# Kernel optimization log

Measured on AMD Instinct MI355X. Metric: run time of the kernel, lower is better.

The kernel has to match this reference:

```python
import jax, jax.numpy as jnp
import numpy as np

EPS = 1e-06


def rotation_trick(e, q):
    # e, q: (..., D). Faithful to torch version, but r_rT @ e and
    # q_hat_e_hatT @ e are algebraically simplified to r*(r.e) and
    # q_hat*(e_hat.e), avoiding the (..., D, D) outer-product tensors.
    sg = jax.lax.stop_gradient
    e_norm = sg(jnp.linalg.norm(e, axis=-1, keepdims=True)) + EPS
    q_norm = sg(jnp.linalg.norm(q, axis=-1, keepdims=True)) + EPS
    e_hat = sg(e / e_norm)
    q_hat = sg(q / q_norm)
    lmbda = q_norm / e_norm
    r = e_hat + q_hat
    r = r / jnp.linalg.norm(r, axis=-1, keepdims=True)
    r_dot_e = jnp.sum(r * e, axis=-1, keepdims=True)
    ehat_dot_e = jnp.sum(e_hat * e, axis=-1, keepdims=True)
    return lmbda * (e - 2.0 * r * r_dot_e + 2.0 * q_hat * ehat_dot_e)


def setup_inputs() -> dict:
    key = jax.random.key(0)
    k1, k2 = jax.random.split(key)
    B, D, H, W = 8, 64, 32, 32
    K = 8192
    x = jax.random.normal(k1, (B, D, H, W), dtype=jnp.float32)
    # init_tensor: L2-normalize uniform rand along dim=1, scale=1
    e = jax.random.uniform(k2, (D, K), dtype=jnp.float32)
    e_i_ts = e / (jnp.linalg.norm(e, axis=1, keepdims=True) + 1e-12)
    return {"x": x, "e_i_ts": e_i_ts}


def reference(x, e_i_ts):
    # x: (B, D, H, W); e_i_ts: (D, K)
    B, D, H, W = x.shape
    x_perm = jnp.transpose(x, (0, 2, 3, 1))          # (B, H, W, D)
    flat_x = x_perm.reshape(-1, D)                   # (N, D)
    distances = (
        jnp.sum(flat_x**2, axis=1, keepdims=True)
        - 2.0 * flat_x @ e_i_ts
        + jnp.sum(e_i_ts**2, axis=0, keepdims=True)
    )                                                # (N, K)
    encoding_indices = jnp.argmin(distances, axis=1) # (N,)
    ind = encoding_indices.reshape(B, H, W)
    quantized_x = e_i_ts.T[ind]                      # (B, H, W, D) gather
    quantized_x_d = rotation_trick(x_perm, quantized_x)
    # permute back to channels-first
    q = jnp.transpose(quantized_x, (0, 3, 1, 2))
    q_d = jnp.transpose(quantized_x_d, (0, 3, 1, 2))
    return (q_d, q, ind)
```

## Files before the change

kernel.cpp:

```cpp
#include <hip/hip_runtime.h>
#include <float.h>
#include <math.h>

#define EPS 1e-6f

typedef __attribute__((ext_vector_type(8))) short short8;
typedef __attribute__((ext_vector_type(4))) float f32x4;

constexpr int Nn = 8192;
constexpr int Dd = 64;
constexpr int Kk = 8192;
constexpr int PLANE = Nn * Dd;
constexpr int KSPLIT = 16;
constexpr int KPB = Kk / KSPLIT;
constexpr int NT = KPB / 16;
constexpr int NPAIR = NT / 2;
constexpr int TILE_USH = 4096;
constexpr int PAIR_BYTES = 2 * TILE_USH * 2;

__device__ __forceinline__ void split3(float v, unsigned short& h1, unsigned short& h2, unsigned short& h3) {
    unsigned u = __float_as_uint(v);
    h1 = (unsigned short)(u >> 16);
    float r1 = v - __uint_as_float((unsigned)h1 << 16);
    h2 = (unsigned short)(__float_as_uint(r1) >> 16);
    float r2 = r1 - __uint_as_float((unsigned)h2 << 16);
    h3 = (unsigned short)(__float_as_uint(r2) >> 16);
}

typedef __attribute__((address_space(3))) unsigned int lds_u32_t;
typedef __attribute__((address_space(1))) unsigned int glb_u32_t;
__device__ __forceinline__ void gload_lds16(const void* g, void* l) {
    __builtin_amdgcn_global_load_lds((const glb_u32_t*)g, (lds_u32_t*)l, 16, 0, 0);
}

__global__ void prep_kernel(const float* __restrict__ e, const float* __restrict__ x,
                            unsigned short* __restrict__ es_t, float* __restrict__ en2h,
                            float* __restrict__ et,
                            unsigned short* __restrict__ xs, float* __restrict__ xn2)
{
    const int tid = threadIdx.x;
    if (blockIdx.x < 32) {
        const int k = blockIdx.x * 256 + tid;
        const int t = k >> 4, l15 = k & 15;
        unsigned short* tb = es_t + (size_t)t * TILE_USH;
        float s = 0.f;
        #pragma unroll
        for (int c = 0; c < 8; ++c) {
            const int ks = c >> 2, kg = c & 3;
            short8 h1v, h2v, h3v;
            float fv[8];
            #pragma unroll
            for (int j = 0; j < 8; ++j) {
                float v = e[(c * 8 + j) * Kk + k];
                fv[j] = v;
                s = fmaf(v, v, s);
                unsigned short h1, h2, h3; split3(v, h1, h2, h3);
                h1v[j] = (short)h1; h2v[j] = (short)h2; h3v[j] = (short)h3;
            }
            const int lofs = (kg * 16 + l15) * 8;
            *(short8*)(tb + (0 * 2 + ks) * 512 + lofs) = h1v;
            *(short8*)(tb + (1 * 2 + ks) * 512 + lofs) = h2v;
            *(short8*)(tb + (2 * 2 + ks) * 512 + lofs) = h3v;
            *(float4*)(et + (size_t)k * Dd + c * 8)     = *(float4*)&fv[0];
            *(float4*)(et + (size_t)k * Dd + c * 8 + 4) = *(float4*)&fv[4];
        }
        unsigned short s1, s2, s3; split3(0.5f * s, s1, s2, s3);
        short8 env = {(short)s1, (short)s2, (short)s3, 0, 0, 0, 0, 0};
        short8 zz  = {0, 0, 0, 0, 0, 0, 0, 0};
        *(short8*)(tb + 6 * 512 + l15 * 8) = env;
        *(short8*)(tb + 6 * 512 + (16 + l15) * 8) = zz;
        *(short8*)(tb + 6 * 512 + (32 + l15) * 8) = zz;
        *(short8*)(tb + 6 * 512 + (48 + l15) * 8) = zz;
        en2h[k] = 0.5f * s;
    } else {
        const int p = (blockIdx.x - 32) * 256 + tid;
        const int b = p >> 10, hw = p & 1023;
        float s = 0.f;
        #pragma unroll
        for (int c = 0; c < 8; ++c) {
            short8 h1v, h2v, h3v;
            #pragma unroll
            for (int j = 0; j < 8; ++j) {
                float v = x[(b * Dd + c * 8 + j) * 1024 + hw];
                s = fmaf(v, v, s);
                unsigned short h1, h2, h3; split3(-v, h1, h2, h3);
                h1v[j] = (short)h1; h2v[j] = (short)h2; h3v[j] = (short)h3;
            }
            *(short8*)(xs + (size_t)p * Dd + c * 8) = h1v;
            *(short8*)(xs + PLANE + (size_t)p * Dd + c * 8) = h2v;
            *(short8*)(xs + 2 * PLANE + (size_t)p * Dd + c * 8) = h3v;
        }
        xn2[p] = s;
    }
}

__device__ __forceinline__ void tile_compute(
    const short8 (&a)[2][3][2], const short8 a_ones, const short8 (&b)[7],
    int nb, int l15, float (&bv)[2][4], int (&bi)[2][4])
{
    const f32x4 zero = {0.f, 0.f, 0.f, 0.f};
    f32x4 acc_en = __builtin_amdgcn_mfma_f32_16x16x32_bf16(a_ones, b[6], zero, 0, 0, 0);
    f32x4 acc[2][2];
    acc[0][0] = acc_en; acc[1][0] = acc_en;
    acc[0][1] = zero;   acc[1][1] = zero;
    #define PROD(sx, se) \
        acc[0][0] = __builtin_amdgcn_mfma_f32_16x16x32_bf16(a[0][sx][0], b[(se)*2+0], acc[0][0], 0,0,0); \
        acc[1][0] = __builtin_amdgcn_mfma_f32_16x16x32_bf16(a[1][sx][0], b[(se)*2+0], acc[1][0], 0,0,0); \
        acc[0][1] = __builtin_amdgcn_mfma_f32_16x16x32_bf16(a[0][sx][1], b[(se)*2+1], acc[0][1], 0,0,0); \
        acc[1][1] = __builtin_amdgcn_mfma_f32_16x16x32_bf16(a[1][sx][1], b[(se)*2+1], acc[1][1], 0,0,0);
    PROD(0,0) PROD(0,1) PROD(1,0) PROD(0,2) PROD(1,1) PROD(2,0)
    #undef PROD
    #pragma unroll
    for (int mi = 0; mi < 2; ++mi)
        #pragma unroll
        for (int j = 0; j < 4; ++j) {
            float s = acc[mi][0][j] + acc[mi][1][j];
            if (s < bv[mi][j]) { bv[mi][j] = s; bi[mi][j] = nb + l15; }
        }
}

__global__ __launch_bounds__(256, 2) void dist_mfma(
    const unsigned short* __restrict__ xs, const unsigned short* __restrict__ es_t,
    float* __restrict__ pval, int* __restrict__ pidx)
{
    __shared__ __align__(16) unsigned short sB[2][2 * TILE_USH];

    const int tid = threadIdx.x;
    const int w = tid >> 6, lane = tid & 63;
    const int l15 = lane & 15, kg = lane >> 4;
    const int m0 = blockIdx.x * 128 + w * 32;
    const int t0 = blockIdx.y * NT;
    const int pr0 = t0 / 2;

    short8 a[2][3][2];
    #pragma unroll
    for (int mi = 0; mi < 2; ++mi) {
        const unsigned short* xp = xs + (size_t)(m0 + mi * 16 + l15) * Dd + kg * 8;
        #pragma unroll
        for (int s = 0; s < 3; ++s)
            #pragma unroll
            for (int ks = 0; ks < 2; ++ks)
                a[mi][s][ks] = *(const short8*)(xp + s * PLANE + ks * 32);
    }
    const short8 a_ones = (kg == 0)
        ? short8{(short)0x3F80, (short)0x3F80, (short)0x3F80, 0, 0, 0, 0, 0}
        : short8{0, 0, 0, 0, 0, 0, 0, 0};

    float bv[2][4]; int bi[2][4];
    #pragma unroll
    for (int mi = 0; mi < 2; ++mi)
        #pragma unroll
        for (int j = 0; j < 4; ++j) { bv[mi][j] = FLT_MAX; bi[mi][j] = 0; }

    #define STAGE_PAIR(buf, pi) { \
        const char* gb_ = (const char*)es_t + (size_t)(pi) * PAIR_BYTES; \
        char* lb_ = (char*)&sB[buf][0]; \
        _Pragma("unroll") \
        for (int r_ = 0; r_ < 4; ++r_) { \
            const int off_ = r_ * 4096 + w * 1024; \
            gload_lds16(gb_ + off_ + lane * 16, lb_ + off_); } }

    STAGE_PAIR(0, pr0)
    asm volatile("s_waitcnt vmcnt(0)" ::: "memory");
    asm volatile("s_barrier" ::: "memory");

    #pragma unroll 1
    for (int pp = 0; pp < NPAIR; ++pp) {
        const int cur = pp & 1;
        const int pn = (pp + 1 < NPAIR) ? pp + 1 : NPAIR - 1;
        STAGE_PAIR(cur ^ 1, pr0 + pn)
        asm volatile("s_waitcnt vmcnt(4)" ::: "memory");
        asm volatile("s_barrier" ::: "memory");

        short8 bf0[7], bf1[7];
        const unsigned short* lb = &sB[cur][lane * 8];
        #pragma unroll
        for (int f = 0; f < 7; ++f) bf0[f] = *(const short8*)(lb + f * 512);
        #pragma unroll
        for (int f = 0; f < 7; ++f) bf1[f] = *(const short8*)(lb + TILE_USH + f * 512);
        asm volatile("s_waitcnt lgkmcnt(0)" ::: "memory");
        asm volatile("s_barrier" ::: "memory");

        const int ti = t0 + pp * 2;
        tile_compute(a, a_ones, bf0, ti * 16, l15, bv, bi);
        tile_compute(a, a_ones, bf1, ti * 16 + 16, l15, bv, bi);
    }

    #pragma unroll
    for (int m = 1; m < 16; m <<= 1) {
        #pragma unroll
        for (int mi = 0; mi < 2; ++mi)
            #pragma unroll
            for (int j = 0; j < 4; ++j) {
                float ov = __shfl_xor(bv[mi][j], m, 64);
                int   oi = __shfl_xor(bi[mi][j], m, 64);
                if (ov < bv[mi][j] || (ov == bv[mi][j] && oi < bi[mi][j])) {
                    bv[mi][j] = ov; bi[mi][j] = oi;
                }
            }
    }
    if (l15 == 0) {
        #pragma unroll
        for (int mi = 0; mi < 2; ++mi)
            #pragma unroll
            for (int j = 0; j < 4; ++j) {
                int pix = m0 + mi * 16 + kg * 4 + j;
                pval[(size_t)pix * KSPLIT + blockIdx.y] = bv[mi][j];
                pidx[(size_t)pix * KSPLIT + blockIdx.y] = bi[mi][j];
            }
    }
}

__global__ __launch_bounds__(256) void finalize_kernel(
    const float* __restrict__ x, const float* __restrict__ et,
    const float* __restrict__ en2h, const float* __restrict__ xn2,
    const float* __restrict__ pval, const int* __restrict__ pidx,
    float* __restrict__ out_qd, float* __restrict__ out_q, float* __restrict__ out_ind)
{
    const int tid = threadIdx.x;
    const int p = blockIdx.x * 256 + tid;

    const float4* pv4 = (const float4*)(pval + (size_t)p * KSPLIT);
    const int4*   pi4 = (const int4*)(pidx + (size_t)p * KSPLIT);
    float bvv = FLT_MAX; int bii = 0;
    #pragma unroll
    for (int u = 0; u < KSPLIT / 4; ++u) {
        float4 v4 = pv4[u]; int4 i4 = pi4[u];
        #pragma unroll
        for (int jj = 0; jj < 4; ++jj) {
            float v = ((const float*)&v4)[jj];
            int   i = ((const int*)&i4)[jj];
            if (v < bvv || (v == bvv && i < bii)) { bvv = v; bii = i; }
        }
    }
    if (blockIdx.y == 0) out_ind[p] = (float)bii;

    float sx2 = xn2[p];
    float enh = en2h[bii];
    float sq2 = 2.f * enh;
    float sxq = enh - bvv;
    float ne = sqrtf(sx2), nq = sqrtf(sq2);
    float inv_e = 1.f / (ne + EPS), inv_q = 1.f / (nq + EPS);
    float lmbda = (nq + EPS) * inv_e;
    float ehat_dot_e = sx2 * inv_e;
    float rn2 = sx2 * inv_e * inv_e + 2.f * sxq * inv_e * inv_q + sq2 * inv_q * inv_q;
    float inv_r = rsqrtf(rn2);
    float rde = (sx2 * inv_e + sxq * inv_q) * inv_r;
    float cx = lmbda * (1.f - 2.f * rde * inv_r * inv_e);
    float cq = 2.f * lmbda * inv_q * (ehat_dot_e - rde * inv_r);

    const int b = p >> 10, hw = p & 1023;
    const int d0 = blockIdx.y * 8;
    const float* xb = x + (b * Dd + d0) * 1024 + hw;
    const float* er = et + (size_t)bii * Dd + d0;
    float* qd_b = out_qd + (b * Dd + d0) * 1024 + hw;
    float* q_b  = out_q  + (b * Dd + d0) * 1024 + hw;
    #pragma unroll
    for (int dv = 0; dv < 2; ++dv) {
        float4 q4 = *(const float4*)(er + dv * 4);
        #pragma unroll
        for (int jj = 0; jj < 4; ++jj) {
            int d = dv * 4 + jj;
            float xv = xb[d * 1024];
            float qv = ((const float*)&q4)[jj];
            qd_b[d * 1024] = cx * xv + cq * qv;
            q_b[d * 1024]  = qv;
        }
    }
}

extern "C" void kernel_launch(void* const* d_in, const int* in_sizes, int n_in,
                              void* d_out, int out_size, void* d_ws, size_t ws_size,
                              hipStream_t stream) {
    const float* x = (const float*)d_in[0];
    const float* e = (const float*)d_in[1];
    float* out = (float*)d_out;
    float* out_qd  = out;
    float* out_q   = out + Nn * Dd;
    float* out_ind = out + 2 * Nn * Dd;

    unsigned short* xs   = (unsigned short*)d_ws;
    unsigned short* es_t = xs + 3 * PLANE;
    float* et   = (float*)(es_t + (size_t)(Kk / 16) * TILE_USH);
    float* en2h = et + (size_t)Kk * Dd;
    float* xn2  = en2h + Kk;
    float* pval = xn2 + Nn;
    int*   pidx = (int*)(pval + (size_t)Nn * KSPLIT);

    prep_kernel<<<64, 256, 0, stream>>>(e, x, es_t, en2h, et, xs, xn2);
    dist_mfma<<<dim3(Nn / 128, KSPLIT), 256, 0, stream>>>(xs, es_t, pval, pidx);
    finalize_kernel<<<dim3(32, 8), 256, 0, stream>>>(x, et, en2h, xn2, pval, pidx,
                                                     out_qd, out_q, out_ind);
}
```

Measured before the change: 65.44 us.

## Split prep into 64-thread e/x kernels and separate coefficient from apply

The combined prep kernel (64 blocks of 256 threads) becomes two kernels with 64-thread blocks, giving 128 blocks each and spreading the work over more CUs. The finalize kernel, which redid the 16-way argmin reduction and the rotation coefficients in each of its 8 channel-slice blocks, is split into a coef kernel that runs once per pixel and an apply kernel that reads the stored coefficients. This removes the redundant reductions and raises prep parallelism, at the cost of two extra launches and a small workspace round trip.

```diff
diff --git a/kernel.cpp b/kernel.cpp
--- a/kernel.cpp
+++ b/kernel.cpp
@@ -33,65 +33,66 @@
     __builtin_amdgcn_global_load_lds((const glb_u32_t*)g, (lds_u32_t*)l, 16, 0, 0);
 }
 
-__global__ void prep_kernel(const float* __restrict__ e, const float* __restrict__ x,
-                            unsigned short* __restrict__ es_t, float* __restrict__ en2h,
-                            float* __restrict__ et,
-                            unsigned short* __restrict__ xs, float* __restrict__ xn2)
-{
-    const int tid = threadIdx.x;
-    if (blockIdx.x < 32) {
-        const int k = blockIdx.x * 256 + tid;
-        const int t = k >> 4, l15 = k & 15;
-        unsigned short* tb = es_t + (size_t)t * TILE_USH;
-        float s = 0.f;
-        #pragma unroll
-        for (int c = 0; c < 8; ++c) {
-            const int ks = c >> 2, kg = c & 3;
-            short8 h1v, h2v, h3v;
-            float fv[8];
-            #pragma unroll
-            for (int j = 0; j < 8; ++j) {
-                float v = e[(c * 8 + j) * Kk + k];
-                fv[j] = v;
-                s = fmaf(v, v, s);
-                unsigned short h1, h2, h3; split3(v, h1, h2, h3);
-                h1v[j] = (short)h1; h2v[j] = (short)h2; h3v[j] = (short)h3;
-            }
-            const int lofs = (kg * 16 + l15) * 8;
-            *(short8*)(tb + (0 * 2 + ks) * 512 + lofs) = h1v;
-            *(short8*)(tb + (1 * 2 + ks) * 512 + lofs) = h2v;
-            *(short8*)(tb + (2 * 2 + ks) * 512 + lofs) = h3v;
-            *(float4*)(et + (size_t)k * Dd + c * 8)     = *(float4*)&fv[0];
-            *(float4*)(et + (size_t)k * Dd + c * 8 + 4) = *(float4*)&fv[4];
-        }
-        unsigned short s1, s2, s3; split3(0.5f * s, s1, s2, s3);
-        short8 env = {(short)s1, (short)s2, (short)s3, 0, 0, 0, 0, 0};
-        short8 zz  = {0, 0, 0, 0, 0, 0, 0, 0};
-        *(short8*)(tb + 6 * 512 + l15 * 8) = env;
-        *(short8*)(tb + 6 * 512 + (16 + l15) * 8) = zz;
-        *(short8*)(tb + 6 * 512 + (32 + l15) * 8) = zz;
-        *(short8*)(tb + 6 * 512 + (48 + l15) * 8) = zz;
-        en2h[k] = 0.5f * s;
-    } else {
-        const int p = (blockIdx.x - 32) * 256 + tid;
-        const int b = p >> 10, hw = p & 1023;
-        float s = 0.f;
-        #pragma unroll
-        for (int c = 0; c < 8; ++c) {
-            short8 h1v, h2v, h3v;
-            #pragma unroll
-            for (int j = 0; j < 8; ++j) {
-                float v = x[(b * Dd + c * 8 + j) * 1024 + hw];
-                s = fmaf(v, v, s);
-                unsigned short h1, h2, h3; split3(-v, h1, h2, h3);
-                h1v[j] = (short)h1; h2v[j] = (short)h2; h3v[j] = (short)h3;
-            }
-            *(short8*)(xs + (size_t)p * Dd + c * 8) = h1v;
-            *(short8*)(xs + PLANE + (size_t)p * Dd + c * 8) = h2v;
-            *(short8*)(xs + 2 * PLANE + (size_t)p * Dd + c * 8) = h3v;
-        }
-        xn2[p] = s;
-    }
+__global__ __launch_bounds__(64) void prep_e_kernel(
+    const float* __restrict__ e, unsigned short* __restrict__ es_t,
+    float* __restrict__ en2h, float* __restrict__ et)
+{
+    const int k = blockIdx.x * 64 + threadIdx.x;
+    const int t = k >> 4, l15 = k & 15;
+    unsigned short* tb = es_t + (size_t)t * TILE_USH;
+    float s = 0.f;
+    #pragma unroll
+    for (int c = 0; c < 8; ++c) {
+        const int ks = c >> 2, kg = c & 3;
+        short8 h1v, h2v, h3v;
+        float fv[8];
+        #pragma unroll
+        for (int j = 0; j < 8; ++j) {
+            float v = e[(c * 8 + j) * Kk + k];
+            fv[j] = v;
+            s = fmaf(v, v, s);
+            unsigned short h1, h2, h3; split3(v, h1, h2, h3);
+            h1v[j] = (short)h1; h2v[j] = (short)h2; h3v[j] = (short)h3;
+        }
+        const int lofs = (kg * 16 + l15) * 8;
+        *(short8*)(tb + (0 * 2 + ks) * 512 + lofs) = h1v;
+        *(short8*)(tb + (1 * 2 + ks) * 512 + lofs) = h2v;
+        *(short8*)(tb + (2 * 2 + ks) * 512 + lofs) = h3v;
+        *(float4*)(et + (size_t)k * Dd + c * 8)     = *(float4*)&fv[0];
+        *(float4*)(et + (size_t)k * Dd + c * 8 + 4) = *(float4*)&fv[4];
+    }
+    unsigned short s1, s2, s3; split3(0.5f * s, s1, s2, s3);
+    short8 env = {(short)s1, (short)s2, (short)s3, 0, 0, 0, 0, 0};
+    short8 zz  = {0, 0, 0, 0, 0, 0, 0, 0};
+    *(short8*)(tb + 6 * 512 + l15 * 8) = env;
+    *(short8*)(tb + 6 * 512 + (16 + l15) * 8) = zz;
+    *(short8*)(tb + 6 * 512 + (32 + l15) * 8) = zz;
+    *(short8*)(tb + 6 * 512 + (48 + l15) * 8) = zz;
+    en2h[k] = 0.5f * s;
+}
+
+__global__ __launch_bounds__(64) void prep_x_kernel(
+    const float* __restrict__ x, unsigned short* __restrict__ xs,
+    float* __restrict__ xn2)
+{
+    const int p = blockIdx.x * 64 + threadIdx.x;
+    const int b = p >> 10, hw = p & 1023;
+    float s = 0.f;
+    #pragma unroll
+    for (int c = 0; c < 8; ++c) {
+        short8 h1v, h2v, h3v;
+        #pragma unroll
+        for (int j = 0; j < 8; ++j) {
+            float v = x[(b * Dd + c * 8 + j) * 1024 + hw];
+            s = fmaf(v, v, s);
+            unsigned short h1, h2, h3; split3(-v, h1, h2, h3);
+            h1v[j] = (short)h1; h2v[j] = (short)h2; h3v[j] = (short)h3;
+        }
+        *(short8*)(xs + (size_t)p * Dd + c * 8) = h1v;
+        *(short8*)(xs + PLANE + (size_t)p * Dd + c * 8) = h2v;
+        *(short8*)(xs + 2 * PLANE + (size_t)p * Dd + c * 8) = h3v;
+    }
+    xn2[p] = s;
 }
 
 __device__ __forceinline__ void tile_compute(
@@ -211,14 +212,13 @@
     }
 }
 
-__global__ __launch_bounds__(256) void finalize_kernel(
-    const float* __restrict__ x, const float* __restrict__ et,
+__global__ __launch_bounds__(256) void coef_kernel(
     const float* __restrict__ en2h, const float* __restrict__ xn2,
     const float* __restrict__ pval, const int* __restrict__ pidx,
-    float* __restrict__ out_qd, float* __restrict__ out_q, float* __restrict__ out_ind)
-{
-    const int tid = threadIdx.x;
-    const int p = blockIdx.x * 256 + tid;
+    float* __restrict__ cxs, float* __restrict__ cqs, int* __restrict__ biis,
+    float* __restrict__ out_ind)
+{
+    const int p = blockIdx.x * 256 + threadIdx.x;
 
     const float4* pv4 = (const float4*)(pval + (size_t)p * KSPLIT);
     const int4*   pi4 = (const int4*)(pidx + (size_t)p * KSPLIT);
@@ -233,7 +233,7 @@
             if (v < bvv || (v == bvv && i < bii)) { bvv = v; bii = i; }
         }
     }
-    if (blockIdx.y == 0) out_ind[p] = (float)bii;
+    out_ind[p] = (float)bii;
 
     float sx2 = xn2[p];
     float enh = en2h[bii];
@@ -246,8 +246,20 @@
     float rn2 = sx2 * inv_e * inv_e + 2.f * sxq * inv_e * inv_q + sq2 * inv_q * inv_q;
     float inv_r = rsqrtf(rn2);
     float rde = (sx2 * inv_e + sxq * inv_q) * inv_r;
-    float cx = lmbda * (1.f - 2.f * rde * inv_r * inv_e);
-    float cq = 2.f * lmbda * inv_q * (ehat_dot_e - rde * inv_r);
+    cxs[p] = lmbda * (1.f - 2.f * rde * inv_r * inv_e);
+    cqs[p] = 2.f * lmbda * inv_q * (ehat_dot_e - rde * inv_r);
+    biis[p] = bii;
+}
+
+__global__ __launch_bounds__(256) void apply_kernel(
+    const float* __restrict__ x, const float* __restrict__ et,
+    const float* __restrict__ cxs, const float* __restrict__ cqs,
+    const int* __restrict__ biis,
+    float* __restrict__ out_qd, float* __restrict__ out_q)
+{
+    const int p = blockIdx.x * 256 + threadIdx.x;
+    const float cx = cxs[p], cq = cqs[p];
+    const int bii = biis[p];
 
     const int b = p >> 10, hw = p & 1023;
     const int d0 = blockIdx.y * 8;
@@ -286,9 +298,13 @@
     float* xn2  = en2h + Kk;
     float* pval = xn2 + Nn;
     int*   pidx = (int*)(pval + (size_t)Nn * KSPLIT);
-
-    prep_kernel<<<64, 256, 0, stream>>>(e, x, es_t, en2h, et, xs, xn2);
+    float* cxs  = (float*)(pidx + (size_t)Nn * KSPLIT);
+    float* cqs  = cxs + Nn;
+    int*   biis = (int*)(cqs + Nn);
+
+    prep_e_kernel<<<Kk / 64, 64, 0, stream>>>(e, es_t, en2h, et);
+    prep_x_kernel<<<Nn / 64, 64, 0, stream>>>(x, xs, xn2);
     dist_mfma<<<dim3(Nn / 128, KSPLIT), 256, 0, stream>>>(xs, es_t, pval, pidx);
-    finalize_kernel<<<dim3(32, 8), 256, 0, stream>>>(x, et, en2h, xn2, pval, pidx,
-                                                     out_qd, out_q, out_ind);
-}
+    coef_kernel<<<Nn / 256, 256, 0, stream>>>(en2h, xn2, pval, pidx, cxs, cqs, biis, out_ind);
+    apply_kernel<<<dim3(Nn / 256, 8), 256, 0, stream>>>(x, et, cxs, cqs, biis, out_qd, out_q);
+}
```

New measurement: 68.79 us. +5.1%, slower.
